# Performance work log

Measured on AMD Instinct MI355X. Metric: run time of the kernel, lower is better.

## Reference

```python
import jax, jax.numpy as jnp
import numpy as np

LN_EPS = 1e-5
N, D = 512, 512


def setup_inputs() -> dict:
    key = jax.random.key(0)
    ks = jax.random.split(key, 3)
    s1 = 1.0 / np.sqrt(2 * D)  # torch Linear default-ish scale
    s2 = 1.0 / np.sqrt(D)
    return {
        "embeddings": jax.random.normal(ks[0], (N, D), jnp.float32),
        "W1": jax.random.normal(ks[1], (2 * D, D), jnp.float32) * s1,  # [in, out]
        "b1": jnp.zeros((D,), jnp.float32),
        "gamma": jnp.ones((D,), jnp.float32),
        "beta": jnp.zeros((D,), jnp.float32),
        "W2": jax.random.normal(ks[2], (D, 1), jnp.float32) * s2,
        "b2": jnp.zeros((1,), jnp.float32),
    }


def reference(embeddings, W1, b1, gamma, beta, W2, b2):
    d = embeddings.shape[-1]
    # Linear(2D -> D) on cat(e_i, e_j) decomposes into two GEMMs + broadcast add,
    # avoiding materializing the [N, N, 2D] concatenated pair tensor.
    left = embeddings @ W1[:d]              # [N, D]  (contribution of e_i)
    right = embeddings @ W1[d:] + b1        # [N, D]  (contribution of e_j + bias)
    h = left[:, None, :] + right[None, :, :]  # [N, N, D]
    # LayerNorm over last dim (eps matches torch default)
    mu = h.mean(axis=-1, keepdims=True)
    var = ((h - mu) ** 2).mean(axis=-1, keepdims=True)
    h = (h - mu) * jax.lax.rsqrt(var + LN_EPS) * gamma + beta
    # exact GELU (torch nn.GELU default)
    h = jax.nn.gelu(h, approximate=False)
    s = jax.nn.sigmoid(jnp.squeeze(h @ W2, -1) + b2[0])  # [N, N]
    # original loop only evaluates pairs i <= j and mirrors to (j, i)
    n = s.shape[0]
    upper = jnp.arange(n)[:, None] <= jnp.arange(n)[None, :]
    return jnp.where(upper, s, s.T)
```

## Files before the change

kernel.cpp:

```cpp
#include <hip/hip_runtime.h>


#define N_ 512
#define D_ 512

__global__ __launch_bounds__(256) void k_gemm(const float* __restrict__ E,
                                              const float* __restrict__ W1,
                                              const float* __restrict__ b1,
                                              float* __restrict__ W ) {
    __shared__ float e[16][516];
    const int t = threadIdx.x;
    const int cc = (blockIdx.x & 7) * 128;
    const int r0 = (blockIdx.x >> 3) * 16;
    const int half = cc >> 9;
    const int c = (cc & 511) + (t & 31) * 4;
    const int rp = (t >> 5) * 2;

    for (int x = t; x < 16 * 128; x += 256) {
        int r = x >> 7, c4 = (x & 127) << 2;
        *(float4*)&e[r][c4] = *(const float4*)&E[(r0 + r) * D_ + c4];
    }
    __syncthreads();

    const float* __restrict__ wp = W1 + (half << 18) + c;
    float4 a0 = {0.f, 0.f, 0.f, 0.f}, a1 = {0.f, 0.f, 0.f, 0.f};
#pragma unroll 4
    for (int k = 0; k < D_; k += 4) {
        float4 e0 = *(float4*)&e[rp][k];
        float4 e1 = *(float4*)&e[rp + 1][k];
        float4 wa = *(const float4*)(wp + ((k + 0) << 9));
        float4 wb = *(const float4*)(wp + ((k + 1) << 9));
        float4 wc = *(const float4*)(wp + ((k + 2) << 9));
        float4 wd = *(const float4*)(wp + ((k + 3) << 9));
        a0.x = fmaf(e0.x, wa.x, a0.x); a0.y = fmaf(e0.x, wa.y, a0.y);
        a0.z = fmaf(e0.x, wa.z, a0.z); a0.w = fmaf(e0.x, wa.w, a0.w);
        a1.x = fmaf(e1.x, wa.x, a1.x); a1.y = fmaf(e1.x, wa.y, a1.y);
        a1.z = fmaf(e1.x, wa.z, a1.z); a1.w = fmaf(e1.x, wa.w, a1.w);
        a0.x = fmaf(e0.y, wb.x, a0.x); a0.y = fmaf(e0.y, wb.y, a0.y);
        a0.z = fmaf(e0.y, wb.z, a0.z); a0.w = fmaf(e0.y, wb.w, a0.w);
        a1.x = fmaf(e1.y, wb.x, a1.x); a1.y = fmaf(e1.y, wb.y, a1.y);
        a1.z = fmaf(e1.y, wb.z, a1.z); a1.w = fmaf(e1.y, wb.w, a1.w);
        a0.x = fmaf(e0.z, wc.x, a0.x); a0.y = fmaf(e0.z, wc.y, a0.y);
        a0.z = fmaf(e0.z, wc.z, a0.z); a0.w = fmaf(e0.z, wc.w, a0.w);
        a1.x = fmaf(e1.z, wc.x, a1.x); a1.y = fmaf(e1.z, wc.y, a1.y);
        a1.z = fmaf(e1.z, wc.z, a1.z); a1.w = fmaf(e1.z, wc.w, a1.w);
        a0.x = fmaf(e0.w, wd.x, a0.x); a0.y = fmaf(e0.w, wd.y, a0.y);
        a0.z = fmaf(e0.w, wd.z, a0.z); a0.w = fmaf(e0.w, wd.w, a0.w);
        a1.x = fmaf(e1.w, wd.x, a1.x); a1.y = fmaf(e1.w, wd.y, a1.y);
        a1.z = fmaf(e1.w, wd.z, a1.z); a1.w = fmaf(e1.w, wd.w, a1.w);
    }
    if (half) {
        float4 bb = *(const float4*)(b1 + c);
        a0.x += bb.x; a0.y += bb.y; a0.z += bb.z; a0.w += bb.w;
        a1.x += bb.x; a1.y += bb.y; a1.z += bb.z; a1.w += bb.w;
    }
    *(float4*)(W + ((half << 9) + r0 + rp) * D_ + c) = a0;
    *(float4*)(W + ((half << 9) + r0 + rp + 1) * D_ + c) = a1;
}

__device__ __forceinline__ float block_sum(float v, float* sred, int t) {
#pragma unroll
    for (int off = 32; off > 0; off >>= 1) v += __shfl_xor(v, off, 64);
    int wave = t >> 6;
    if ((t & 63) == 0) sred[wave] = v;
    __syncthreads();
    float s = sred[0] + sred[1] + sred[2] + sred[3];
    __syncthreads();
    return s;
}

__global__ __launch_bounds__(256) void k_center(float* __restrict__ W,
                                                float* __restrict__ var) {
    __shared__ float sred[4];
    const int r = blockIdx.x, t = threadIdx.x;
    float* p = W + r * D_;
    float v0 = p[t], v1 = p[t + 256];
    float s = block_sum(v0 + v1, sred, t);
    float mean = s * (1.f / D_);
    float c0 = v0 - mean, c1 = v1 - mean;
    float ss = block_sum(c0 * c0 + c1 * c1, sred, t);
    p[t] = c0;
    p[t + 256] = c1;
    if (t == 0) var[r] = ss * (1.f / D_);
}

__device__ __forceinline__ void gelu_acc(float l, float r, float g, float be,
                                         float w, float rstd, float& acc) {
    float s = l + r;
    float x = fmaf(s * rstd, g, be);
    float x2 = x * x;
    float q = x * fmaf(-0.10294340f, x2, -2.30220935f);
    float eq = __builtin_amdgcn_exp2f(q);
    float ge = x * __builtin_amdgcn_rcpf(1.f + eq);
    acc = fmaf(ge, w, acc);
}

__global__ __launch_bounds__(256) void k_pair(const float* __restrict__ W,
                                              const float* __restrict__ var,
                                              const float* __restrict__ gf,
                                              const float* __restrict__ bef,
                                              const float* __restrict__ wf,
                                              const float* __restrict__ b2f,
                                              float* __restrict__ out) {
    __shared__ float ls[16][260];
    __shared__ float rs[16][260];
    __shared__ float red[4096];
    __shared__ float rstd_s[256];

    const int b = blockIdx.x;
    int I = (int)((65.0f - sqrtf(4225.0f - 8.0f * (float)b)) * 0.5f);
    if (I < 0) I = 0;
    if (I > 31) I = 31;
#define S_(i) (32 * (i) - ((i) * ((i)-1)) / 2)
    while (S_(I) > b) --I;
    while (S_(I + 1) <= b) ++I;
    const int J = I + (b - S_(I));
#undef S_

    const int t = threadIdx.x;
    const int ks = t & 15, pt = t >> 4;
    const int i4 = (pt & 3) * 4, j4 = (pt >> 2) * 4;
    const int Ibase = I * 16, Jbase = N_ + J * 16;

    float cv[16];
#pragma unroll
    for (int c = 0; c < 16; ++c) cv[c] = 0.f;
    for (int kb = 0; kb < D_; kb += 256) {
        for (int x = t; x < 16 * 64; x += 256) {
            int r = x >> 6, c4 = (x & 63) << 2;
            *(float4*)&ls[r][c4] = *(const float4*)&W[(Ibase + r) * D_ + kb + c4];
            *(float4*)&rs[r][c4] = *(const float4*)&W[(Jbase + r) * D_ + kb + c4];
        }
        __syncthreads();
#pragma unroll
        for (int it = 0; it < 4; ++it) {
            const int kq = (it * 16 + ks) * 4;
            float4 lq[4], rq[4];
#pragma unroll
            for (int d = 0; d < 4; ++d) {
                lq[d] = *(float4*)&ls[i4 + d][kq];
                rq[d] = *(float4*)&rs[j4 + d][kq];
            }
#pragma unroll
            for (int di = 0; di < 4; ++di)
#pragma unroll
                for (int dj = 0; dj < 4; ++dj)
                    cv[di * 4 + dj] += lq[di].x * rq[dj].x + lq[di].y * rq[dj].y +
                                       lq[di].z * rq[dj].z + lq[di].w * rq[dj].w;
        }
        __syncthreads();
    }
#pragma unroll
    for (int c = 0; c < 16; ++c) red[ks * 256 + pt * 16 + c] = cv[c];
    __syncthreads();

    const int ri = t >> 4, rj = t & 15;
    const int rpt = (ri >> 2) + ((rj >> 2) << 2);
    const int rc = (ri & 3) * 4 + (rj & 3);
    {
        float cov = 0.f;
#pragma unroll
        for (int k2 = 0; k2 < 16; ++k2) cov += red[k2 * 256 + rpt * 16 + rc];
        float varh = var[Ibase + ri] + var[Jbase + rj] + cov * (2.f / D_) + 1e-5f;
        rstd_s[t] = rsqrtf(varh);
    }
    __syncthreads();

    float rst[16];
#pragma unroll
    for (int di = 0; di < 4; ++di)
#pragma unroll
        for (int dj = 0; dj < 4; ++dj)
            rst[di * 4 + dj] = rstd_s[(i4 + di) * 16 + (j4 + dj)];
    float ac[16];
#pragma unroll
    for (int c = 0; c < 16; ++c) ac[c] = 0.f;
    for (int kb = 0; kb < D_; kb += 256) {
        for (int x = t; x < 16 * 64; x += 256) {
            int r = x >> 6, c4 = (x & 63) << 2;
            *(float4*)&ls[r][c4] = *(const float4*)&W[(Ibase + r) * D_ + kb + c4];
            *(float4*)&rs[r][c4] = *(const float4*)&W[(Jbase + r) * D_ + kb + c4];
        }
        __syncthreads();
#pragma unroll
        for (int it = 0; it < 4; ++it) {
            const int kq = (it * 16 + ks) * 4;
            float4 g4 = *(const float4*)&gf[kb + kq];
            float4 be4 = *(const float4*)&bef[kb + kq];
            float4 w4 = *(const float4*)&wf[kb + kq];
            float4 lq[4], rq[4];
#pragma unroll
            for (int d = 0; d < 4; ++d) {
                lq[d] = *(float4*)&ls[i4 + d][kq];
                rq[d] = *(float4*)&rs[j4 + d][kq];
            }
#pragma unroll
            for (int di = 0; di < 4; ++di)
#pragma unroll
                for (int dj = 0; dj < 4; ++dj) {
                    float rr = rst[di * 4 + dj];
                    float& a = ac[di * 4 + dj];
                    gelu_acc(lq[di].x, rq[dj].x, g4.x, be4.x, w4.x, rr, a);
                    gelu_acc(lq[di].y, rq[dj].y, g4.y, be4.y, w4.y, rr, a);
                    gelu_acc(lq[di].z, rq[dj].z, g4.z, be4.z, w4.z, rr, a);
                    gelu_acc(lq[di].w, rq[dj].w, g4.w, be4.w, w4.w, rr, a);
                }
        }
        __syncthreads();
    }
#pragma unroll
    for (int c = 0; c < 16; ++c) red[ks * 256 + pt * 16 + c] = ac[c];
    __syncthreads();

    {
        float z = b2f[0];
#pragma unroll
        for (int k2 = 0; k2 < 16; ++k2) z += red[k2 * 256 + rpt * 16 + rc];
        float sg = __builtin_amdgcn_rcpf(1.f + __builtin_amdgcn_exp2f(-1.44269504f * z));
        const int gi = Ibase + ri, gj = (Jbase - N_) + rj;
        if (gi <= gj) {
            out[gi * N_ + gj] = sg;
            out[gj * N_ + gi] = sg;
        }
    }
}

extern "C" void kernel_launch(void* const* d_in, const int* in_sizes, int n_in,
                              void* d_out, int out_size, void* d_ws, size_t ws_size,
                              hipStream_t stream) {
    const float* E     = (const float*)d_in[0];
    const float* W1    = (const float*)d_in[1];
    const float* b1    = (const float*)d_in[2];
    const float* gamma = (const float*)d_in[3];
    const float* beta  = (const float*)d_in[4];
    const float* w2    = (const float*)d_in[5];
    const float* b2    = (const float*)d_in[6];
    float* out = (float*)d_out;

    float* F    = (float*)d_ws;
    float* lcrc = F;
    float* var  = F + 1024 * 512;

    k_gemm<<<256, 256, 0, stream>>>(E, W1, b1, lcrc);
    k_center<<<1024, 256, 0, stream>>>(lcrc, var);
    k_pair<<<528, 256, 0, stream>>>(lcrc, var, gamma, beta, w2, b2, out);
}
```

Measured before the change: 131.7 us.

## Restructure pair kernel to 512 threads with full-row smem and shuffle reductions

The pair kernel now loads the full 512-wide rows for the 16x16 tile into shared memory once, instead of reloading them twice per K-half. It also runs 512 threads with 2x4 outputs each and replaces the shared-memory partial-sum reductions with intra-wave shuffles, which removes the red buffer and most barriers. Off-diagonal tiles write the output with vectorized stores, and k_center processes one row per wavefront with float4 loads and shuffle-only reductions. The trade-offs are larger shared memory per block, which may limit occupancy, and a doubled thread count that could add register pressure.

```diff
diff --git a/kernel.cpp b/kernel.cpp
--- a/kernel.cpp
+++ b/kernel.cpp
@@ -58,30 +58,27 @@
     *(float4*)(W + ((half << 9) + r0 + rp + 1) * D_ + c) = a1;
 }
 
-__device__ __forceinline__ float block_sum(float v, float* sred, int t) {
-#pragma unroll
-    for (int off = 32; off > 0; off >>= 1) v += __shfl_xor(v, off, 64);
-    int wave = t >> 6;
-    if ((t & 63) == 0) sred[wave] = v;
-    __syncthreads();
-    float s = sred[0] + sred[1] + sred[2] + sred[3];
-    __syncthreads();
-    return s;
-}
-
 __global__ __launch_bounds__(256) void k_center(float* __restrict__ W,
                                                 float* __restrict__ var) {
-    __shared__ float sred[4];
-    const int r = blockIdx.x, t = threadIdx.x;
+    const int t = threadIdx.x;
+    const int lane = t & 63;
+    const int r = (blockIdx.x << 2) + (t >> 6);
     float* p = W + r * D_;
-    float v0 = p[t], v1 = p[t + 256];
-    float s = block_sum(v0 + v1, sred, t);
-    float mean = s * (1.f / D_);
-    float c0 = v0 - mean, c1 = v1 - mean;
-    float ss = block_sum(c0 * c0 + c1 * c1, sred, t);
-    p[t] = c0;
-    p[t + 256] = c1;
-    if (t == 0) var[r] = ss * (1.f / D_);
+    float4 v0 = *(float4*)&p[lane << 2];
+    float4 v1 = *(float4*)&p[256 + (lane << 2)];
+    float s = (v0.x + v0.y) + (v0.z + v0.w) + (v1.x + v1.y) + (v1.z + v1.w);
+#pragma unroll
+    for (int off = 32; off > 0; off >>= 1) s += __shfl_xor(s, off, 64);
+    const float mean = s * (1.f / D_);
+    v0.x -= mean; v0.y -= mean; v0.z -= mean; v0.w -= mean;
+    v1.x -= mean; v1.y -= mean; v1.z -= mean; v1.w -= mean;
+    float ss = v0.x * v0.x + v0.y * v0.y + v0.z * v0.z + v0.w * v0.w +
+               v1.x * v1.x + v1.y * v1.y + v1.z * v1.z + v1.w * v1.w;
+#pragma unroll
+    for (int off = 32; off > 0; off >>= 1) ss += __shfl_xor(ss, off, 64);
+    *(float4*)&p[lane << 2] = v0;
+    *(float4*)&p[256 + (lane << 2)] = v1;
+    if (lane == 0) var[r] = ss * (1.f / D_);
 }
 
 __device__ __forceinline__ void gelu_acc(float l, float r, float g, float be,
@@ -95,17 +92,15 @@
     acc = fmaf(ge, w, acc);
 }
 
-__global__ __launch_bounds__(256) void k_pair(const float* __restrict__ W,
-                                              const float* __restrict__ var,
-                                              const float* __restrict__ gf,
-                                              const float* __restrict__ bef,
-                                              const float* __restrict__ wf,
-                                              const float* __restrict__ b2f,
-                                              float* __restrict__ out) {
-    __shared__ float ls[16][260];
-    __shared__ float rs[16][260];
-    __shared__ float red[4096];
-    __shared__ float rstd_s[256];
+__global__ __launch_bounds__(512, 4) void k_pair(const float* __restrict__ W,
+                                                 const float* __restrict__ var,
+                                                 const float* __restrict__ gf,
+                                                 const float* __restrict__ bef,
+                                                 const float* __restrict__ wf,
+                                                 const float* __restrict__ b2f,
+                                                 float* __restrict__ out) {
+    __shared__ float ls[16][516];
+    __shared__ float rs[16][516];
 
     const int b = blockIdx.x;
     int I = (int)((65.0f - sqrtf(4225.0f - 8.0f * (float)b)) * 0.5f);
@@ -118,109 +113,130 @@
 #undef S_
 
     const int t = threadIdx.x;
-    const int ks = t & 15, pt = t >> 4;
-    const int i4 = (pt & 3) * 4, j4 = (pt >> 2) * 4;
+    const int ks = t & 15;
+    const int pt = t >> 4;
+    const int i2 = (pt & 7) * 2, j4 = (pt >> 3) * 4;
     const int Ibase = I * 16, Jbase = N_ + J * 16;
 
-    float cv[16];
-#pragma unroll
-    for (int c = 0; c < 16; ++c) cv[c] = 0.f;
-    for (int kb = 0; kb < D_; kb += 256) {
-        for (int x = t; x < 16 * 64; x += 256) {
-            int r = x >> 6, c4 = (x & 63) << 2;
-            *(float4*)&ls[r][c4] = *(const float4*)&W[(Ibase + r) * D_ + kb + c4];
-            *(float4*)&rs[r][c4] = *(const float4*)&W[(Jbase + r) * D_ + kb + c4];
+    for (int x = t; x < 16 * 128; x += 512) {
+        int r = x >> 7, c4 = (x & 127) << 2;
+        *(float4*)&ls[r][c4] = *(const float4*)&W[(Ibase + r) * D_ + c4];
+        *(float4*)&rs[r][c4] = *(const float4*)&W[(Jbase + r) * D_ + c4];
+    }
+    __syncthreads();
+
+    float cv[8];
+#pragma unroll
+    for (int c = 0; c < 8; ++c) cv[c] = 0.f;
+#pragma unroll
+    for (int it = 0; it < 8; ++it) {
+        const int kq = (it * 16 + ks) * 4;
+        float4 lq[2], rq[4];
+#pragma unroll
+        for (int d = 0; d < 2; ++d) lq[d] = *(float4*)&ls[i2 + d][kq];
+#pragma unroll
+        for (int d = 0; d < 4; ++d) rq[d] = *(float4*)&rs[j4 + d][kq];
+#pragma unroll
+        for (int di = 0; di < 2; ++di)
+#pragma unroll
+            for (int dj = 0; dj < 4; ++dj)
+                cv[di * 4 + dj] += lq[di].x * rq[dj].x + lq[di].y * rq[dj].y +
+                                   lq[di].z * rq[dj].z + lq[di].w * rq[dj].w;
+    }
+#pragma unroll
+    for (int c = 0; c < 8; ++c) {
+        float v = cv[c];
+        v += __shfl_xor(v, 1, 64);
+        v += __shfl_xor(v, 2, 64);
+        v += __shfl_xor(v, 4, 64);
+        v += __shfl_xor(v, 8, 64);
+        cv[c] = v;
+    }
+
+    float rst[8];
+    {
+        float vl[2], vr[4];
+#pragma unroll
+        for (int d = 0; d < 2; ++d) vl[d] = var[Ibase + i2 + d];
+#pragma unroll
+        for (int d = 0; d < 4; ++d) vr[d] = var[Jbase - N_ + N_ + j4 + d];
+#pragma unroll
+        for (int di = 0; di < 2; ++di)
+#pragma unroll
+            for (int dj = 0; dj < 4; ++dj)
+                rst[di * 4 + dj] =
+                    rsqrtf(vl[di] + vr[dj] + cv[di * 4 + dj] * (2.f / D_) + 1e-5f);
+    }
+
+    float ac[8];
+#pragma unroll
+    for (int c = 0; c < 8; ++c) ac[c] = 0.f;
+#pragma unroll 2
+    for (int it = 0; it < 8; ++it) {
+        const int kq = (it * 16 + ks) * 4;
+        float4 g4 = *(const float4*)&gf[kq];
+        float4 be4 = *(const float4*)&bef[kq];
+        float4 w4 = *(const float4*)&wf[kq];
+        float4 lq[2], rq[4];
+#pragma unroll
+        for (int d = 0; d < 2; ++d) lq[d] = *(float4*)&ls[i2 + d][kq];
+#pragma unroll
+        for (int d = 0; d < 4; ++d) rq[d] = *(float4*)&rs[j4 + d][kq];
+#pragma unroll
+        for (int di = 0; di < 2; ++di)
+#pragma unroll
+            for (int dj = 0; dj < 4; ++dj) {
+                float rr = rst[di * 4 + dj];
+                float& a = ac[di * 4 + dj];
+                gelu_acc(lq[di].x, rq[dj].x, g4.x, be4.x, w4.x, rr, a);
+                gelu_acc(lq[di].y, rq[dj].y, g4.y, be4.y, w4.y, rr, a);
+                gelu_acc(lq[di].z, rq[dj].z, g4.z, be4.z, w4.z, rr, a);
+                gelu_acc(lq[di].w, rq[dj].w, g4.w, be4.w, w4.w, rr, a);
+            }
+    }
+#pragma unroll
+    for (int c = 0; c < 8; ++c) {
+        float v = ac[c];
+        v += __shfl_xor(v, 1, 64);
+        v += __shfl_xor(v, 2, 64);
+        v += __shfl_xor(v, 4, 64);
+        v += __shfl_xor(v, 8, 64);
+        ac[c] = v;
+    }
+
+    if (ks == 0) {
+        const float bb = b2f[0];
+        float z[8];
+#pragma unroll
+        for (int c = 0; c < 8; ++c) {
+            float zz = ac[c] + bb;
+            z[c] = __builtin_amdgcn_rcpf(
+                1.f + __builtin_amdgcn_exp2f(-1.44269504f * zz));
         }
-        __syncthreads();
-#pragma unroll
-        for (int it = 0; it < 4; ++it) {
-            const int kq = (it * 16 + ks) * 4;
-            float4 lq[4], rq[4];
-#pragma unroll
-            for (int d = 0; d < 4; ++d) {
-                lq[d] = *(float4*)&ls[i4 + d][kq];
-                rq[d] = *(float4*)&rs[j4 + d][kq];
+        const int gi0 = Ibase + i2;
+        const int gj0 = (Jbase - N_) + j4;
+        if (I < J) {
+            float4 o0 = {z[0], z[1], z[2], z[3]};
+            float4 o1 = {z[4], z[5], z[6], z[7]};
+            *(float4*)&out[gi0 * N_ + gj0] = o0;
+            *(float4*)&out[(gi0 + 1) * N_ + gj0] = o1;
+#pragma unroll
+            for (int dj = 0; dj < 4; ++dj) {
+                out[(gj0 + dj) * N_ + gi0] = z[dj];
+                out[(gj0 + dj) * N_ + gi0 + 1] = z[4 + dj];
             }
-#pragma unroll
-            for (int di = 0; di < 4; ++di)
-#pragma unroll
-                for (int dj = 0; dj < 4; ++dj)
-                    cv[di * 4 + dj] += lq[di].x * rq[dj].x + lq[di].y * rq[dj].y +
-                                       lq[di].z * rq[dj].z + lq[di].w * rq[dj].w;
-        }
-        __syncthreads();
-    }
-#pragma unroll
-    for (int c = 0; c < 16; ++c) red[ks * 256 + pt * 16 + c] = cv[c];
-    __syncthreads();
-
-    const int ri = t >> 4, rj = t & 15;
-    const int rpt = (ri >> 2) + ((rj >> 2) << 2);
-    const int rc = (ri & 3) * 4 + (rj & 3);
-    {
-        float cov = 0.f;
-#pragma unroll
-        for (int k2 = 0; k2 < 16; ++k2) cov += red[k2 * 256 + rpt * 16 + rc];
-        float varh = var[Ibase + ri] + var[Jbase + rj] + cov * (2.f / D_) + 1e-5f;
-        rstd_s[t] = rsqrtf(varh);
-    }
-    __syncthreads();
-
-    float rst[16];
-#pragma unroll
-    for (int di = 0; di < 4; ++di)
-#pragma unroll
-        for (int dj = 0; dj < 4; ++dj)
-            rst[di * 4 + dj] = rstd_s[(i4 + di) * 16 + (j4 + dj)];
-    float ac[16];
-#pragma unroll
-    for (int c = 0; c < 16; ++c) ac[c] = 0.f;
-    for (int kb = 0; kb < D_; kb += 256) {
-        for (int x = t; x < 16 * 64; x += 256) {
-            int r = x >> 6, c4 = (x & 63) << 2;
-            *(float4*)&ls[r][c4] = *(const float4*)&W[(Ibase + r) * D_ + kb + c4];
-            *(float4*)&rs[r][c4] = *(const float4*)&W[(Jbase + r) * D_ + kb + c4];
-        }
-        __syncthreads();
-#pragma unroll
-        for (int it = 0; it < 4; ++it) {
-            const int kq = (it * 16 + ks) * 4;
-            float4 g4 = *(const float4*)&gf[kb + kq];
-            float4 be4 = *(const float4*)&bef[kb + kq];
-            float4 w4 = *(const float4*)&wf[kb + kq];
-            float4 lq[4], rq[4];
-#pragma unroll
-            for (int d = 0; d < 4; ++d) {
-                lq[d] = *(float4*)&ls[i4 + d][kq];
-                rq[d] = *(float4*)&rs[j4 + d][kq];
-            }
-#pragma unroll
-            for (int di = 0; di < 4; ++di)
+        } else {
+#pragma unroll
+            for (int di = 0; di < 2; ++di)
 #pragma unroll
                 for (int dj = 0; dj < 4; ++dj) {
-                    float rr = rst[di * 4 + dj];
-                    float& a = ac[di * 4 + dj];
-                    gelu_acc(lq[di].x, rq[dj].x, g4.x, be4.x, w4.x, rr, a);
-                    gelu_acc(lq[di].y, rq[dj].y, g4.y, be4.y, w4.y, rr, a);
-                    gelu_acc(lq[di].z, rq[dj].z, g4.z, be4.z, w4.z, rr, a);
-                    gelu_acc(lq[di].w, rq[dj].w, g4.w, be4.w, w4.w, rr, a);
+                    int gi = gi0 + di, gj = gj0 + dj;
+                    if (gi <= gj) {
+                        float zz = z[di * 4 + dj];
+                        out[gi * N_ + gj] = zz;
+                        out[gj * N_ + gi] = zz;
+                    }
                 }
-        }
-        __syncthreads();
-    }
-#pragma unroll
-    for (int c = 0; c < 16; ++c) red[ks * 256 + pt * 16 + c] = ac[c];
-    __syncthreads();
-
-    {
-        float z = b2f[0];
-#pragma unroll
-        for (int k2 = 0; k2 < 16; ++k2) z += red[k2 * 256 + rpt * 16 + rc];
-        float sg = __builtin_amdgcn_rcpf(1.f + __builtin_amdgcn_exp2f(-1.44269504f * z));
-        const int gi = Ibase + ri, gj = (Jbase - N_) + rj;
-        if (gi <= gj) {
-            out[gi * N_ + gj] = sg;
-            out[gj * N_ + gi] = sg;
         }
     }
 }
@@ -242,6 +258,6 @@
     float* var  = F + 1024 * 512;
 
     k_gemm<<<256, 256, 0, stream>>>(E, W1, b1, lcrc);
-    k_center<<<1024, 256, 0, stream>>>(lcrc, var);
-    k_pair<<<528, 256, 0, stream>>>(lcrc, var, gamma, beta, w2, b2, out);
-}
+    k_center<<<256, 256, 0, stream>>>(lcrc, var);
+    k_pair<<<528, 512, 0, stream>>>(lcrc, var, gamma, beta, w2, b2, out);
+}
```

Result: slower. 138.5 us (+5.2%).
